# Kernel tuning notes

Hardware: AMD Instinct MI355X
Metric: run time of the kernel (lower is better)

Reference implementation:

```python
import jax, jax.numpy as jnp
import numpy as np

B, C, H, W = 8, 128, 128, 128
R = 4
K = 2 * R + 1  # 9 -> 81 correlation channels


def conv2d(x, w, pad=0):
    return jax.lax.conv_general_dilated(
        x, w, (1, 1), [(pad, pad), (pad, pad)],
        dimension_numbers=('NCHW', 'OIHW', 'NCHW'))


def group_norm(x, gamma, beta, groups, eps=1e-5):
    b, c, h, w = x.shape
    xr = x.reshape(b, groups, c // groups, h, w)
    m = xr.mean(axis=(2, 3, 4), keepdims=True)
    v = ((xr - m) ** 2).mean(axis=(2, 3, 4), keepdims=True)
    xn = ((xr - m) * jax.lax.rsqrt(v + eps)).reshape(b, c, h, w)
    return xn * gamma[None, :, None, None] + beta[None, :, None, None]


def bilinear_warp(x, flow):
    # torch grid_sample(mode=bilinear, padding_mode=zeros, align_corners=True)
    # with vgrid = grid + flow normalized then un-normalized -> pixel coords = grid + flow
    b, c, h, w = x.shape
    px = jnp.arange(w, dtype=flow.dtype)[None, None, :] + flow[:, 0]  # [B,H,W]
    py = jnp.arange(h, dtype=flow.dtype)[None, :, None] + flow[:, 1]
    x0 = jnp.floor(px)
    y0 = jnp.floor(py)
    wx = px - x0
    wy = py - y0

    def sample_one(img, x0, y0, wx, wy):
        def corner(xi, yi):
            valid = ((xi >= 0) & (xi <= w - 1) & (yi >= 0) & (yi <= h - 1)).astype(img.dtype)
            xc = jnp.clip(xi, 0, w - 1).astype(jnp.int32)
            yc = jnp.clip(yi, 0, h - 1).astype(jnp.int32)
            return img[:, yc, xc] * valid[None]  # [C,H,W]
        return (corner(x0, y0) * ((1 - wx) * (1 - wy))[None]
                + corner(x0 + 1, y0) * (wx * (1 - wy))[None]
                + corner(x0, y0 + 1) * ((1 - wx) * wy)[None]
                + corner(x0 + 1, y0 + 1) * (wx * wy)[None])

    return jax.vmap(sample_one)(x, x0, y0, wx, wy)


def cost_volume(f1, f2):
    # 81 shifted windows of zero-padded f2, channel-mean correlation with f1
    b, c, h, w = f1.shape
    pad = jnp.pad(f2, ((0, 0), (0, 0), (R, R), (R, R)))
    vols = [(f1 * jax.lax.slice(pad, (0, 0, y, x), (b, c, y + h, x + w))).mean(axis=1)
            for y in range(K) for x in range(K)]
    return jnp.stack(vols, axis=1)  # [B, 81, H, W]


def _forward(feat1, feat2, p):
    x = conv2d(jnp.concatenate([feat1, feat2], axis=1), p['off_w1'], 1)
    x = jax.nn.silu(group_norm(x, p['off_g1'], p['off_b1'], 32))
    x = conv2d(x, p['off_w2'], 1)
    x = jax.nn.silu(group_norm(x, p['off_g2'], p['off_b2'], 32))
    pred = conv2d(x, p['off_w3'], 1) + p['off_bias3'][None, :, None, None]
    flow = pred[:, :2]
    validity = jax.nn.sigmoid(pred[:, 2:3])
    aligned = bilinear_warp(feat2, flow) * validity
    cv = cost_volume(feat1, aligned)
    diff = jnp.abs(feat1 - aligned)
    ce = jax.nn.relu(group_norm(conv2d(cv, p['corr_w']), p['corr_g'], p['corr_b'], 32))
    de = jax.nn.relu(group_norm(conv2d(diff, p['diff_w']), p['diff_g'], p['diff_b'], 32))
    f = conv2d(jnp.concatenate([ce, de], axis=1), p['fus_w1'], 1)
    f = jax.nn.relu(group_norm(f, p['fus_g1'], p['fus_b1'], 32))
    f = conv2d(f, p['fus_w2'])
    lam = jax.nn.sigmoid(conv2d(f, p['lam_w']) + p['lam_b'][None, :, None, None])
    return aligned, flow, lam


def setup_inputs() -> dict:
    key = jax.random.key(0)
    ks = jax.random.split(key, 12)

    def cw(k, oc, ic, kk, scale=None):
        s = np.float32(np.sqrt(2.0 / (oc * kk * kk))) if scale is None else np.float32(scale)
        return jax.random.normal(k, (oc, ic, kk, kk), jnp.float32) * s

    return {
        'feat1': jax.random.normal(ks[0], (B, C, H, W), jnp.float32),
        'feat2': jax.random.normal(ks[1], (B, C, H, W), jnp.float32),
        'off_w1': cw(ks[2], C, 2 * C, 3),
        'off_g1': jnp.ones((C,), jnp.float32), 'off_b1': jnp.zeros((C,), jnp.float32),
        'off_w2': cw(ks[3], C // 2, C, 3),
        'off_g2': jnp.ones((C // 2,), jnp.float32), 'off_b2': jnp.zeros((C // 2,), jnp.float32),
        'off_w3': cw(ks[4], 3, C // 2, 3, 0.01),  # original inits to zero; small random for nontrivial flow
        'off_bias3': jnp.array([0.0, 0.0, 2.0], jnp.float32),  # bias[2]=2.0 as in _init_weights
        'corr_w': cw(ks[5], C // 2, K * K, 1),
        'corr_g': jnp.ones((C // 2,), jnp.float32), 'corr_b': jnp.zeros((C // 2,), jnp.float32),
        'diff_w': cw(ks[6], C // 2, C, 1),
        'diff_g': jnp.ones((C // 2,), jnp.float32), 'diff_b': jnp.zeros((C // 2,), jnp.float32),
        'fus_w1': cw(ks[7], C, C, 3),
        'fus_g1': jnp.ones((C,), jnp.float32), 'fus_b1': jnp.zeros((C,), jnp.float32),
        'fus_w2': cw(ks[8], C, C, 1),
        'lam_w': cw(ks[9], 1, C, 1),
        'lam_b': jnp.zeros((1,), jnp.float32),
    }


def reference(feat1, feat2, off_w1, off_g1, off_b1, off_w2, off_g2, off_b2, off_w3, off_bias3,
              corr_w, corr_g, corr_b, diff_w, diff_g, diff_b,
              fus_w1, fus_g1, fus_b1, fus_w2, lam_w, lam_b):
    p = dict(off_w1=off_w1, off_g1=off_g1, off_b1=off_b1, off_w2=off_w2, off_g2=off_g2,
             off_b2=off_b2, off_w3=off_w3, off_bias3=off_bias3, corr_w=corr_w, corr_g=corr_g,
             corr_b=corr_b, diff_w=diff_w, diff_g=diff_g, diff_b=diff_b, fus_w1=fus_w1,
             fus_g1=fus_g1, fus_b1=fus_b1, fus_w2=fus_w2, lam_w=lam_w, lam_b=lam_b)
    return _forward(feat1, feat2, p)
```

## Files before the change

### kernel.cpp

```cpp
#include <hip/hip_runtime.h>
#include <math.h>

#define BATCH 8
#define H 128
#define W 128
#define HW 16384

typedef short bf16x8 __attribute__((ext_vector_type(8)));
typedef float f32x16 __attribute__((ext_vector_type(16)));
typedef unsigned int u32;
typedef unsigned short u16;

__device__ __forceinline__ u16 f2bf(float v) {
    u32 u = __float_as_uint(v);
    u = (u + 0x7fffu + ((u >> 16) & 1u)) >> 16;
    return (u16)u;
}

__device__ __forceinline__ void async16(void* lds, const void* g) {
    __builtin_amdgcn_global_load_lds(
        (const __attribute__((address_space(1))) u32*)g,
        (__attribute__((address_space(3))) u32*)lds, 16, 0, 0);
}

__global__ __launch_bounds__(256) void wtrans_kernel(
    const float* __restrict__ w, float* __restrict__ wt, int O, int I, int KK)
{
    int idx = blockIdx.x * 256 + threadIdx.x;
    int total = O * I * KK;
    if (idx >= total) return;
    int k = idx % KK;
    int rest = idx / KK;
    int i = rest % I;
    int o = rest / I;
    wt[(i * KK + k) * O + o] = w[idx];
}

__global__ void wc_kernel(const float* __restrict__ fus_w2,
                          const float* __restrict__ lam_w,
                          float* __restrict__ wc)
{
    int ic = threadIdx.x;
    float s = 0.f;
    for (int oc = 0; oc < 128; ++oc) s += lam_w[oc] * fus_w2[oc * 128 + ic];
    wc[ic] = s;
}

__global__ __launch_bounds__(256) void wprep_kernel(
    const float* __restrict__ w, u16* __restrict__ out, int Cin, int Cout)
{
    int idx = blockIdx.x * 256 + threadIdx.x;
    int total = Cin * 9 * Cout;
    if (idx >= total) return;
    int ocblks = Cout >> 6;
    int pair = idx / 9216;
    int r = idx - pair * 9216;
    int half = r / 4608;
    int r2 = r - half * 4608;
    int kidx = r2 / 512;
    int r3 = r2 - kidx * 512;
    int oc = r3 >> 3;
    int ic8 = r3 & 7;
    int icblk = pair / ocblks;
    int ocblk = pair - icblk * ocblks;
    int ic = icblk * 16 + half * 8 + ic8;
    int o = ocblk * 64 + oc;
    int ky = kidx / 3, kx = kidx - ky * 3;
    out[idx] = f2bf(w[((size_t)(o * Cin + ic) * 3 + ky) * 3 + kx]);
}

__global__ __launch_bounds__(256) void nhwc_concat_kernel(
    const float* __restrict__ f1, const float* __restrict__ f2,
    u16* __restrict__ out)
{
    __shared__ u16 s[32 * 256];
    int tid = threadIdx.x;
    int b = blockIdx.y;
    int xt = blockIdx.x & 3;
    int y = blockIdx.x >> 2;
    int x0 = xt * 32;
    for (int e = tid; e < 8192; e += 256) {
        int c = e >> 5, px = e & 31;
        const float* src = (c < 128) ? f1 + ((size_t)(b * 128 + c)) * HW
                                     : f2 + ((size_t)(b * 128 + c - 128)) * HW;
        s[px * 256 + c] = f2bf(src[y * W + x0 + px]);
    }
    __syncthreads();
    uint4* o4 = (uint4*)(out + (((size_t)b * 130 + y + 1) * 130 + x0 + 1) * 256);
    const uint4* s4 = (const uint4*)s;
    for (int e = tid; e < 1024; e += 256) o4[e] = s4[e];
}

__global__ __launch_bounds__(256) void gn_nhwc_kernel(
    const float* __restrict__ x, const float* __restrict__ gamma,
    const float* __restrict__ beta, const float* __restrict__ stats,
    u16* __restrict__ out, int Csrc, int Cdst, int coff, int Cg, int act)
{
    __shared__ u16 s[32 * 128];
    int tid = threadIdx.x;
    int b = blockIdx.y;
    int xt = blockIdx.x & 3;
    int y = blockIdx.x >> 2;
    int x0 = xt * 32;
    int n = 32 * Csrc;
    for (int e = tid; e < n; e += 256) {
        int c = e >> 5, px = e & 31;
        float v = x[((size_t)(b * Csrc + c)) * HW + y * W + x0 + px];
        int g = c / Cg;
        float mean = stats[(b * 32 + g) * 2];
        float rstd = stats[(b * 32 + g) * 2 + 1];
        float t = (v - mean) * rstd * gamma[c] + beta[c];
        t = (act == 1) ? t / (1.f + expf(-t)) : fmaxf(t, 0.f);
        s[px * Csrc + c] = f2bf(t);
    }
    __syncthreads();
    int cpp = Csrc >> 3;
    int chunks = 32 * cpp;
    for (int e = tid; e < chunks; e += 256) {
        int px = e / cpp, g = e - px * cpp;
        uint4 v = *(const uint4*)&s[px * Csrc + g * 8];
        *(uint4*)&out[(((size_t)b * 130 + y + 1) * 130 + x0 + 1 + px) * Cdst + coff + g * 8] = v;
    }
}

__global__ __launch_bounds__(256, 2) void conv3x3_mfma_kernel(
    const u16* __restrict__ in_nhwc, const u16* __restrict__ wprep,
    float* __restrict__ out, int Cin, int Cout)
{
    __shared__ u16 s_in[2 * 10 * 34 * 8];
    __shared__ u16 s_w[2 * 9 * 64 * 8];

    const int tid = threadIdx.x;
    const int b = blockIdx.y;
    const int x0 = (blockIdx.x & 3) * 32;
    const int y0 = (blockIdx.x >> 2) * 8;
    const int oc0 = blockIdx.z * 64;
    const int ocblks = Cout >> 6;
    const int icblks = Cin >> 4;

    const int lane = tid & 63;
    const int wv = tid >> 6;
    const int m = lane & 31;
    const int hh = lane >> 5;

    f32x16 acc[2][2];
#pragma unroll
    for (int t = 0; t < 2; ++t)
#pragma unroll
        for (int nt = 0; nt < 2; ++nt)
#pragma unroll
            for (int k = 0; k < 16; ++k) acc[t][nt][k] = 0.f;

    const u16* wsrc0 = wprep + (size_t)blockIdx.z * 9216;

    for (int it = 0; it < icblks; ++it) {
        const int ic0 = it * 16;
        __syncthreads();
        for (int e = tid; e < 680; e += 256) {
            int half = (e >= 340);
            int p = e - half * 340;
            int r = p / 34;
            int col = p - r * 34;
            const u16* src = in_nhwc +
                (((size_t)(b * 130 + y0 + r)) * 130 + (x0 + col)) * Cin + ic0 + half * 8;
            async16(&s_in[e * 8], src);
        }
        const u16* wsrc = wsrc0 + (size_t)it * ocblks * 9216;
        for (int e = tid; e < 1152; e += 256)
            async16(&s_w[e * 8], wsrc + e * 8);
        __syncthreads();

#pragma unroll
        for (int kidx = 0; kidx < 9; ++kidx) {
            const int dy = kidx / 3, dx = kidx - dy * 3;
            bf16x8 a0 = *(const bf16x8*)&s_in[(hh * 340 + (wv * 2 + 0 + dy) * 34 + m + dx) * 8];
            bf16x8 a1 = *(const bf16x8*)&s_in[(hh * 340 + (wv * 2 + 1 + dy) * 34 + m + dx) * 8];
            bf16x8 b0 = *(const bf16x8*)&s_w[(hh * 576 + kidx * 64 + m) * 8];
            bf16x8 b1 = *(const bf16x8*)&s_w[(hh * 576 + kidx * 64 + 32 + m) * 8];
            acc[0][0] = __builtin_amdgcn_mfma_f32_32x32x16_bf16(a0, b0, acc[0][0], 0, 0, 0);
            acc[0][1] = __builtin_amdgcn_mfma_f32_32x32x16_bf16(a0, b1, acc[0][1], 0, 0, 0);
            acc[1][0] = __builtin_amdgcn_mfma_f32_32x32x16_bf16(a1, b0, acc[1][0], 0, 0, 0);
            acc[1][1] = __builtin_amdgcn_mfma_f32_32x32x16_bf16(a1, b1, acc[1][1], 0, 0, 0);
        }
    }

#pragma unroll
    for (int t = 0; t < 2; ++t) {
        int y = y0 + wv * 2 + t;
#pragma unroll
        for (int nt = 0; nt < 2; ++nt) {
            int oc = oc0 + nt * 32 + m;
            float* op = out + ((size_t)(b * Cout + oc)) * HW + y * W + x0;
#pragma unroll
            for (int g = 0; g < 4; ++g) {
                float4 v = make_float4(acc[t][nt][g * 4 + 0], acc[t][nt][g * 4 + 1],
                                       acc[t][nt][g * 4 + 2], acc[t][nt][g * 4 + 3]);
                *(float4*)(op + g * 8 + hh * 4) = v;
            }
        }
    }
}

#define CK 8
__global__ __launch_bounds__(256) void conv3x3_kernel(
    const float* __restrict__ in0, int C0,
    const float* __restrict__ in1, int C1,
    const float* __restrict__ wt,
    const float* __restrict__ bias,
    float* __restrict__ out, int Cout)
{
    __shared__ alignas(16) float s_in[CK][6][36];
    __shared__ alignas(16) float s_w[CK][9][32];

    int b = blockIdx.y;
    int octile = blockIdx.z * 32;
    int tile = blockIdx.x;
    int x0 = (tile & 3) * 32;
    int y0 = (tile >> 2) * 4;
    int tid = threadIdx.x;
    int oc4 = (tid & 7) * 4;
    int pg = tid >> 3;
    int tyy = pg >> 3;
    int txx = (pg & 7) * 4;
    int Cin = C0 + C1;

    float acc[4][4];
#pragma unroll
    for (int j = 0; j < 4; ++j)
#pragma unroll
        for (int o = 0; o < 4; ++o) acc[j][o] = 0.f;

    for (int cb = 0; cb < Cin; cb += CK) {
        __syncthreads();
        for (int e = tid; e < CK * 6 * 34; e += 256) {
            int cc = e / 204;
            int rem = e - cc * 204;
            int r = rem / 34;
            int col = rem - r * 34;
            int gy = y0 + r - 1;
            int gx = x0 + col - 1;
            float v = 0.f;
            if (gy >= 0 && gy < H && gx >= 0 && gx < W) {
                int c = cb + cc;
                v = (c < C0) ? in0[((size_t)b * C0 + c) * HW + gy * W + gx]
                             : in1[((size_t)b * C1 + (c - C0)) * HW + gy * W + gx];
            }
            s_in[cc][r][col] = v;
        }
        for (int e = tid; e < CK * 9 * 32; e += 256) {
            int cc = e / 288;
            int rem = e - cc * 288;
            int k = rem / 32;
            int oc = rem - k * 32;
            int gc = octile + oc;
            s_w[cc][k][oc] = (gc < Cout) ? wt[((size_t)(cb + cc) * 9 + k) * Cout + gc] : 0.f;
        }
        __syncthreads();

#pragma unroll
        for (int cc = 0; cc < CK; ++cc) {
            float xin[3][6];
#pragma unroll
            for (int i = 0; i < 3; ++i) {
                const float4 v4 = *(const float4*)&s_in[cc][tyy + i][txx];
                const float2 v2 = *(const float2*)&s_in[cc][tyy + i][txx + 4];
                xin[i][0] = v4.x; xin[i][1] = v4.y; xin[i][2] = v4.z; xin[i][3] = v4.w;
                xin[i][4] = v2.x; xin[i][5] = v2.y;
            }
#pragma unroll
            for (int ky = 0; ky < 3; ++ky)
#pragma unroll
                for (int kx = 0; kx < 3; ++kx) {
                    const float4 wvv = *(const float4*)&s_w[cc][ky * 3 + kx][oc4];
#pragma unroll
                    for (int j = 0; j < 4; ++j) {
                        float xv = xin[ky][j + kx];
                        acc[j][0] += wvv.x * xv;
                        acc[j][1] += wvv.y * xv;
                        acc[j][2] += wvv.z * xv;
                        acc[j][3] += wvv.w * xv;
                    }
                }
        }
    }

    int ox = x0 + txx;
    int oy = y0 + tyy;
#pragma unroll
    for (int o = 0; o < 4; ++o) {
        int oc = octile + oc4 + o;
        if (oc < Cout) {
            float bv = bias ? bias[oc] : 0.f;
            float4 vv = make_float4(acc[0][o] + bv, acc[1][o] + bv,
                                    acc[2][o] + bv, acc[3][o] + bv);
            *(float4*)&out[((size_t)b * Cout + oc) * HW + oy * W + ox] = vv;
        }
    }
}

__global__ __launch_bounds__(256) void gn_stats_kernel(
    const float* __restrict__ x, float* __restrict__ stats, int CgHW)
{
    int bg = blockIdx.x;
    const float4* p4 = (const float4*)(x + (size_t)bg * CgHW);
    int n4 = CgHW / 4;
    float s1 = 0.f, s2 = 0.f;
    for (int i = threadIdx.x; i < n4; i += 256) {
        float4 v = p4[i];
        s1 += v.x + v.y + v.z + v.w;
        s2 += v.x * v.x + v.y * v.y + v.z * v.z + v.w * v.w;
    }
    for (int off = 32; off > 0; off >>= 1) {
        s1 += __shfl_down(s1, off);
        s2 += __shfl_down(s2, off);
    }
    __shared__ float r1[4], r2[4];
    int wid = threadIdx.x >> 6;
    if ((threadIdx.x & 63) == 0) { r1[wid] = s1; r2[wid] = s2; }
    __syncthreads();
    if (threadIdx.x == 0) {
        float a = r1[0] + r1[1] + r1[2] + r1[3];
        float q = r2[0] + r2[1] + r2[2] + r2[3];
        float inv_n = 1.0f / (float)CgHW;
        float mean = a * inv_n;
        float var = q * inv_n - mean * mean;
        stats[bg * 2] = mean;
        stats[bg * 2 + 1] = rsqrtf(var + 1e-5f);
    }
}

__global__ __launch_bounds__(256) void gn_norm_act_kernel(
    const float* __restrict__ x, float* __restrict__ y,
    const float* __restrict__ gamma, const float* __restrict__ beta,
    const float* __restrict__ stats, int C, int Cg, int act)
{
    int idx = blockIdx.x * 256 + threadIdx.x;
    int total4 = BATCH * C * HW / 4;
    if (idx >= total4) return;
    int e = idx * 4;
    int c = (e / HW) % C;
    int b = e / (C * HW);
    int g = c / Cg;
    float mean = stats[(b * 32 + g) * 2];
    float rstd = stats[(b * 32 + g) * 2 + 1];
    float sc = rstd * gamma[c];
    float sh = beta[c] - mean * sc;
    float4 v = ((const float4*)x)[idx];
    float r[4] = {v.x, v.y, v.z, v.w};
#pragma unroll
    for (int i = 0; i < 4; ++i) {
        float t = r[i] * sc + sh;
        if (act == 1) t = t / (1.f + expf(-t));
        else if (act == 2) t = fmaxf(t, 0.f);
        r[i] = t;
    }
    ((float4*)y)[idx] = make_float4(r[0], r[1], r[2], r[3]);
}

__global__ __launch_bounds__(256) void warp_kernel(
    const float* __restrict__ feat2, const float* __restrict__ pred,
    float* __restrict__ aligned, float* __restrict__ flow_out)
{
    int idx = blockIdx.x * 256 + threadIdx.x;
    int b = idx / HW;
    int p = idx - b * HW;
    int y = p >> 7;
    int x = p & 127;
    const float* predb = pred + (size_t)b * 3 * HW;
    float fx = predb[p];
    float fy = predb[HW + p];
    float validity = 1.f / (1.f + expf(-predb[2 * HW + p]));
    flow_out[(size_t)(b * 2) * HW + p] = fx;
    flow_out[(size_t)(b * 2 + 1) * HW + p] = fy;

    float px = (float)x + fx;
    float py = (float)y + fy;
    float x0f = floorf(px), y0f = floorf(py);
    float wx = px - x0f, wy = py - y0f;
    int xi0 = (int)x0f, yi0 = (int)y0f;
    float wgt[2][2] = {{(1.f - wx) * (1.f - wy), wx * (1.f - wy)},
                       {(1.f - wx) * wy, wx * wy}};
    float vm[2][2];
    int offc[2][2];
#pragma unroll
    for (int yy = 0; yy < 2; ++yy)
#pragma unroll
        for (int xx = 0; xx < 2; ++xx) {
            int xi = xi0 + xx, yi = yi0 + yy;
            bool ok = (xi >= 0) && (xi <= W - 1) && (yi >= 0) && (yi <= H - 1);
            vm[yy][xx] = ok ? wgt[yy][xx] : 0.f;
            int xc = min(max(xi, 0), W - 1);
            int yc = min(max(yi, 0), H - 1);
            offc[yy][xx] = yc * W + xc;
        }
    const float* f2b = feat2 + (size_t)b * 128 * HW;
    float* outb = aligned + (size_t)b * 128 * HW;
    for (int c = 0; c < 128; ++c) {
        const float* f2c = f2b + (size_t)c * HW;
        float val = f2c[offc[0][0]] * vm[0][0] + f2c[offc[0][1]] * vm[0][1] +
                    f2c[offc[1][0]] * vm[1][0] + f2c[offc[1][1]] * vm[1][1];
        outb[(size_t)c * HW + p] = val * validity;
    }
}

__global__ __launch_bounds__(256) void costvol_kernel(
    const float* __restrict__ feat1, const float* __restrict__ aligned,
    float* __restrict__ cv)
{
    __shared__ alignas(16) float s_al[24 * 24 * 4];
    int b = blockIdx.y;
    int bx = blockIdx.x & 7, by = blockIdx.x >> 3;
    int tid = threadIdx.x;
    int ly = tid >> 4, lx = tid & 15;
    int gy = by * 16 + ly, gx = bx * 16 + lx;

    float acc[81];
#pragma unroll
    for (int k = 0; k < 81; ++k) acc[k] = 0.f;

    const float* f1b = feat1 + (size_t)b * 128 * HW;
    const float* alb = aligned + (size_t)b * 128 * HW;

    for (int c0 = 0; c0 < 128; c0 += 4) {
        __syncthreads();
        for (int e = tid; e < 24 * 24 * 4; e += 256) {
            int cc = e / 576;
            int rem = e - cc * 576;
            int r = rem / 24;
            int col = rem - r * 24;
            int ay = by * 16 + r - 4, ax = bx * 16 + col - 4;
            float v = 0.f;
            if (ay >= 0 && ay < H && ax >= 0 && ax < W)
                v = alb[(size_t)(c0 + cc) * HW + ay * W + ax];
            s_al[(r * 24 + col) * 4 + cc] = v;
        }
        __syncthreads();
        float f1v[4];
#pragma unroll
        for (int cc = 0; cc < 4; ++cc)
            f1v[cc] = f1b[(size_t)(c0 + cc) * HW + gy * W + gx];
#pragma unroll
        for (int dy = 0; dy < 9; ++dy) {
#pragma unroll
            for (int dx = 0; dx < 9; ++dx) {
                const float4 av = *(const float4*)&s_al[((ly + dy) * 24 + lx + dx) * 4];
                acc[dy * 9 + dx] += av.x * f1v[0] + av.y * f1v[1] + av.z * f1v[2] + av.w * f1v[3];
            }
        }
    }
    const float scale = 1.f / 128.f;
    float* cvb = cv + (size_t)b * 81 * HW + gy * W + gx;
#pragma unroll
    for (int k = 0; k < 81; ++k) cvb[(size_t)k * HW] = acc[k] * scale;
}

__global__ __launch_bounds__(256) void conv1x1_kernel(
    const float* __restrict__ inA, const float* __restrict__ inB,
    const float* __restrict__ wt, float* __restrict__ out, int Cin)
{
    __shared__ alignas(16) float s_w[128 * 64];
    int tid = threadIdx.x;
    for (int e = tid; e < Cin * 64; e += 256) s_w[e] = wt[e];
    __syncthreads();
    int idx = blockIdx.x * 256 + tid;
    int b = idx / HW;
    int p = idx - b * HW;
    float acc[64];
#pragma unroll
    for (int o = 0; o < 64; ++o) acc[o] = 0.f;
    const float* Ab = inA + (size_t)b * Cin * HW + p;
    const float* Bb = inB ? inB + (size_t)b * Cin * HW + p : nullptr;
    for (int ic = 0; ic < Cin; ++ic) {
        float xv = Ab[(size_t)ic * HW];
        if (inB) xv = fabsf(xv - Bb[(size_t)ic * HW]);
        const float* wr = &s_w[ic * 64];
#pragma unroll
        for (int o4 = 0; o4 < 64; o4 += 4) {
            const float4 wvv = *(const float4*)&wr[o4];
            acc[o4 + 0] += wvv.x * xv;
            acc[o4 + 1] += wvv.y * xv;
            acc[o4 + 2] += wvv.z * xv;
            acc[o4 + 3] += wvv.w * xv;
        }
    }
    float* ob = out + (size_t)b * 64 * HW + p;
#pragma unroll
    for (int o = 0; o < 64; ++o) ob[(size_t)o * HW] = acc[o];
}

__global__ __launch_bounds__(256) void lam_kernel(
    const float* __restrict__ f1, const float* __restrict__ wc,
    const float* __restrict__ lam_b, float* __restrict__ out)
{
    __shared__ float s_w[128];
    int tid = threadIdx.x;
    if (tid < 128) s_w[tid] = wc[tid];
    __syncthreads();
    int idx = blockIdx.x * 256 + tid;
    int b = idx / HW;
    int p = idx - b * HW;
    const float* fb = f1 + (size_t)b * 128 * HW + p;
    float acc = 0.f;
#pragma unroll 4
    for (int ic = 0; ic < 128; ++ic) acc += s_w[ic] * fb[(size_t)ic * HW];
    acc += lam_b[0];
    out[idx] = 1.f / (1.f + expf(-acc));
}

extern "C" void kernel_launch(void* const* d_in, const int* in_sizes, int n_in,
                              void* d_out, int out_size, void* d_ws, size_t ws_size,
                              hipStream_t stream)
{
    const float* feat1     = (const float*)d_in[0];
    const float* feat2     = (const float*)d_in[1];
    const float* off_w1    = (const float*)d_in[2];
    const float* off_g1    = (const float*)d_in[3];
    const float* off_b1    = (const float*)d_in[4];
    const float* off_w2    = (const float*)d_in[5];
    const float* off_g2    = (const float*)d_in[6];
    const float* off_b2    = (const float*)d_in[7];
    const float* off_w3    = (const float*)d_in[8];
    const float* off_bias3 = (const float*)d_in[9];
    const float* corr_w    = (const float*)d_in[10];
    const float* corr_g    = (const float*)d_in[11];
    const float* corr_b    = (const float*)d_in[12];
    const float* diff_w    = (const float*)d_in[13];
    const float* diff_g    = (const float*)d_in[14];
    const float* diff_b    = (const float*)d_in[15];
    const float* fus_w1    = (const float*)d_in[16];
    const float* fus_g1    = (const float*)d_in[17];
    const float* fus_b1    = (const float*)d_in[18];
    const float* fus_w2    = (const float*)d_in[19];
    const float* lam_w     = (const float*)d_in[20];
    const float* lam_b     = (const float*)d_in[21];

    float* ws = (float*)d_ws;
    float* x1  = ws;
    float* x2  = ws + 16777216;
    float* Rcv = ws + 25165824;
    float* Rp1 = ws + 35782656;
    u16*  wp1u = (u16*)(ws + 53088256);
    u16*  wp2u = (u16*)(ws + 53235712);
    u16*  wpfu = (u16*)(ws + 53272576);
    float* wT3 = ws + 53346304;
    float* wTc = ws + 53348032;
    float* wTd = ws + 53353216;
    float* wcb = ws + 53361408;
    float* st  = ws + 53361536;

    u16* p1u = (u16*)Rp1;
    u16* p2u = (u16*)Rcv;
    u16* pfu = (u16*)Rcv;
    float* cv = Rcv;
    float* ce = Rp1;
    float* pred = Rp1 + 8388608;

    float* aligned  = (float*)d_out;
    float* flow_out = aligned + 16777216;
    float* lam_out  = aligned + 17039360;

    auto T = [&](const float* w, float* wt, int O, int I, int KK) {
        int total = O * I * KK;
        hipLaunchKernelGGL(wtrans_kernel, dim3((total + 255) / 256), dim3(256), 0, stream,
                           w, wt, O, I, KK);
    };
    T(off_w3, wT3, 3, 64, 9);
    T(corr_w, wTc, 64, 81, 1);
    T(diff_w, wTd, 64, 128, 1);
    hipLaunchKernelGGL(wc_kernel, dim3(1), dim3(128), 0, stream, fus_w2, lam_w, wcb);
    hipLaunchKernelGGL(wprep_kernel, dim3(1152), dim3(256), 0, stream, off_w1, wp1u, 256, 128);
    hipLaunchKernelGGL(wprep_kernel, dim3(288), dim3(256), 0, stream, off_w2, wp2u, 128, 64);
    hipLaunchKernelGGL(wprep_kernel, dim3(576), dim3(256), 0, stream, fus_w1, wpfu, 128, 128);

    hipMemsetAsync(p1u, 0, (size_t)34611200 * 2, stream);
    hipMemsetAsync(p2u, 0, (size_t)17305600 * 2, stream);

    hipLaunchKernelGGL(nhwc_concat_kernel, dim3(512, 8), dim3(256), 0, stream,
                       feat1, feat2, p1u);
    hipLaunchKernelGGL(conv3x3_mfma_kernel, dim3(64, 8, 2), dim3(256), 0, stream,
                       p1u, wp1u, x1, 256, 128);
    hipLaunchKernelGGL(gn_stats_kernel, dim3(256), dim3(256), 0, stream, x1, st, 65536);
    hipLaunchKernelGGL(gn_nhwc_kernel, dim3(512, 8), dim3(256), 0, stream,
                       x1, off_g1, off_b1, st, p2u, 128, 128, 0, 4, 1);
    hipLaunchKernelGGL(conv3x3_mfma_kernel, dim3(64, 8, 1), dim3(256), 0, stream,
                       p2u, wp2u, x2, 128, 64);
    hipLaunchKernelGGL(gn_stats_kernel, dim3(256), dim3(256), 0, stream, x2, st + 512, 32768);
    hipLaunchKernelGGL(gn_norm_act_kernel, dim3(8192), dim3(256), 0, stream,
                       x2, x2, off_g2, off_b2, st + 512, 64, 2, 1);
    hipLaunchKernelGGL(conv3x3_kernel, dim3(128, 8, 1), dim3(256), 0, stream,
                       x2, 64, (const float*)nullptr, 0, wT3, off_bias3, pred, 3);

    hipLaunchKernelGGL(warp_kernel, dim3(512), dim3(256), 0, stream,
                       feat2, pred, aligned, flow_out);
    hipLaunchKernelGGL(costvol_kernel, dim3(64, 8), dim3(256), 0, stream,
                       feat1, aligned, cv);

    hipLaunchKernelGGL(conv1x1_kernel, dim3(512), dim3(256), 0, stream,
                       cv, (const float*)nullptr, wTc, ce, 81);
    hipLaunchKernelGGL(gn_stats_kernel, dim3(256), dim3(256), 0, stream, ce, st + 1024, 32768);
    hipMemsetAsync(pfu, 0, (size_t)17305600 * 2, stream);
    hipLaunchKernelGGL(gn_nhwc_kernel, dim3(512, 8), dim3(256), 0, stream,
                       ce, corr_g, corr_b, st + 1024, pfu, 64, 128, 0, 2, 2);

    hipLaunchKernelGGL(conv1x1_kernel, dim3(512), dim3(256), 0, stream,
                       feat1, aligned, wTd, x2, 128);
    hipLaunchKernelGGL(gn_stats_kernel, dim3(256), dim3(256), 0, stream, x2, st + 1536, 32768);
    hipLaunchKernelGGL(gn_nhwc_kernel, dim3(512, 8), dim3(256), 0, stream,
                       x2, diff_g, diff_b, st + 1536, pfu, 64, 128, 64, 2, 2);

    hipLaunchKernelGGL(conv3x3_mfma_kernel, dim3(64, 8, 2), dim3(256), 0, stream,
                       pfu, wpfu, x1, 128, 128);
    hipLaunchKernelGGL(gn_stats_kernel, dim3(256), dim3(256), 0, stream, x1, st + 2048, 65536);
    hipLaunchKernelGGL(gn_norm_act_kernel, dim3(16384), dim3(256), 0, stream,
                       x1, x1, fus_g1, fus_b1, st + 2048, 128, 4, 2);
    hipLaunchKernelGGL(lam_kernel, dim3(512), dim3(256), 0, stream,
                       x1, wcb, lam_b, lam_out);
}
```

Before: 1.096 ms.

## Enlarge conv tiles with register reuse, bf16 cost volume, border-only zeroing

The MFMA 3x3 conv now computes 16 output rows per block instead of 8. Each wave loads its 6x3 input fragments into registers once and reuses them across the 9 kernel taps and 4 row tiles. The cost volume packs 8 channels per pixel as bf16 in LDS, halving LDS traffic per channel, at the cost of reduced precision in the correlation. Full-buffer memsets of the padded NHWC buffers are replaced by a kernel that zeroes only the 1-pixel border, which avoids writing the whole buffer but relies on the interior being fully overwritten.

```diff
diff --git a/kernel.cpp b/kernel.cpp
--- a/kernel.cpp
+++ b/kernel.cpp
@@ -69,6 +69,26 @@
     out[idx] = f2bf(w[((size_t)(o * Cin + ic) * 3 + ky) * 3 + kx]);
 }
 
+__global__ __launch_bounds__(256) void border_zero_kernel(u16* __restrict__ buf, int C)
+{
+    int chunks = 516 * C / 8;
+    int idx = blockIdx.x * 256 + threadIdx.x;
+    int total = BATCH * chunks;
+    if (idx >= total) return;
+    int b = idx / chunks;
+    int r = idx - b * chunks;
+    int e = r * 8;
+    int pix = e / C;
+    int co = e - pix * C;
+    int y, x;
+    if (pix < 130)      { y = 0;   x = pix; }
+    else if (pix < 260) { y = 129; x = pix - 130; }
+    else if (pix < 388) { y = 1 + (pix - 260); x = 0; }
+    else                { y = 1 + (pix - 388); x = 129; }
+    uint4 z = make_uint4(0u, 0u, 0u, 0u);
+    *(uint4*)&buf[(((size_t)b * 130 + y) * 130 + x) * C + co] = z;
+}
+
 __global__ __launch_bounds__(256) void nhwc_concat_kernel(
     const float* __restrict__ f1, const float* __restrict__ f2,
     u16* __restrict__ out)
@@ -127,13 +147,13 @@
     const u16* __restrict__ in_nhwc, const u16* __restrict__ wprep,
     float* __restrict__ out, int Cin, int Cout)
 {
-    __shared__ u16 s_in[2 * 10 * 34 * 8];
+    __shared__ u16 s_in[2 * 18 * 34 * 8];
     __shared__ u16 s_w[2 * 9 * 64 * 8];
 
     const int tid = threadIdx.x;
     const int b = blockIdx.y;
     const int x0 = (blockIdx.x & 3) * 32;
-    const int y0 = (blockIdx.x >> 2) * 8;
+    const int y0 = (blockIdx.x >> 2) * 16;
     const int oc0 = blockIdx.z * 64;
     const int ocblks = Cout >> 6;
     const int icblks = Cin >> 4;
@@ -143,9 +163,9 @@
     const int m = lane & 31;
     const int hh = lane >> 5;
 
-    f32x16 acc[2][2];
-#pragma unroll
-    for (int t = 0; t < 2; ++t)
+    f32x16 acc[4][2];
+#pragma unroll
+    for (int t = 0; t < 4; ++t)
 #pragma unroll
         for (int nt = 0; nt < 2; ++nt)
 #pragma unroll
@@ -156,9 +176,9 @@
     for (int it = 0; it < icblks; ++it) {
         const int ic0 = it * 16;
         __syncthreads();
-        for (int e = tid; e < 680; e += 256) {
-            int half = (e >= 340);
-            int p = e - half * 340;
+        for (int e = tid; e < 1224; e += 256) {
+            int half = (e >= 612);
+            int p = e - half * 612;
             int r = p / 34;
             int col = p - r * 34;
             const u16* src = in_nhwc +
@@ -170,23 +190,29 @@
             async16(&s_w[e * 8], wsrc + e * 8);
         __syncthreads();
 
+        bf16x8 a[6][3];
+#pragma unroll
+        for (int s = 0; s < 6; ++s)
+#pragma unroll
+            for (int d = 0; d < 3; ++d)
+                a[s][d] = *(const bf16x8*)&s_in[(hh * 612 + (wv * 4 + s) * 34 + m + d) * 8];
+
 #pragma unroll
         for (int kidx = 0; kidx < 9; ++kidx) {
             const int dy = kidx / 3, dx = kidx - dy * 3;
-            bf16x8 a0 = *(const bf16x8*)&s_in[(hh * 340 + (wv * 2 + 0 + dy) * 34 + m + dx) * 8];
-            bf16x8 a1 = *(const bf16x8*)&s_in[(hh * 340 + (wv * 2 + 1 + dy) * 34 + m + dx) * 8];
             bf16x8 b0 = *(const bf16x8*)&s_w[(hh * 576 + kidx * 64 + m) * 8];
             bf16x8 b1 = *(const bf16x8*)&s_w[(hh * 576 + kidx * 64 + 32 + m) * 8];
-            acc[0][0] = __builtin_amdgcn_mfma_f32_32x32x16_bf16(a0, b0, acc[0][0], 0, 0, 0);
-            acc[0][1] = __builtin_amdgcn_mfma_f32_32x32x16_bf16(a0, b1, acc[0][1], 0, 0, 0);
-            acc[1][0] = __builtin_amdgcn_mfma_f32_32x32x16_bf16(a1, b0, acc[1][0], 0, 0, 0);
-            acc[1][1] = __builtin_amdgcn_mfma_f32_32x32x16_bf16(a1, b1, acc[1][1], 0, 0, 0);
-        }
-    }
-
-#pragma unroll
-    for (int t = 0; t < 2; ++t) {
-        int y = y0 + wv * 2 + t;
+#pragma unroll
+            for (int t = 0; t < 4; ++t) {
+                acc[t][0] = __builtin_amdgcn_mfma_f32_32x32x16_bf16(a[t + dy][dx], b0, acc[t][0], 0, 0, 0);
+                acc[t][1] = __builtin_amdgcn_mfma_f32_32x32x16_bf16(a[t + dy][dx], b1, acc[t][1], 0, 0, 0);
+            }
+        }
+    }
+
+#pragma unroll
+    for (int t = 0; t < 4; ++t) {
+        int y = y0 + wv * 4 + t;
 #pragma unroll
         for (int nt = 0; nt < 2; ++nt) {
             int oc = oc0 + nt * 32 + m;
@@ -403,11 +429,11 @@
     }
 }
 
-__global__ __launch_bounds__(256) void costvol_kernel(
+__global__ __launch_bounds__(256, 1) void costvol_kernel(
     const float* __restrict__ feat1, const float* __restrict__ aligned,
     float* __restrict__ cv)
 {
-    __shared__ alignas(16) float s_al[24 * 24 * 4];
+    __shared__ u16 s_al[576 * 8];
     int b = blockIdx.y;
     int bx = blockIdx.x & 7, by = blockIdx.x >> 3;
     int tid = threadIdx.x;
@@ -421,30 +447,46 @@
     const float* f1b = feat1 + (size_t)b * 128 * HW;
     const float* alb = aligned + (size_t)b * 128 * HW;
 
-    for (int c0 = 0; c0 < 128; c0 += 4) {
+    for (int c0 = 0; c0 < 128; c0 += 8) {
         __syncthreads();
-        for (int e = tid; e < 24 * 24 * 4; e += 256) {
-            int cc = e / 576;
-            int rem = e - cc * 576;
-            int r = rem / 24;
-            int col = rem - r * 24;
+        for (int e = tid; e < 576; e += 256) {
+            int r = e / 24;
+            int col = e - r * 24;
             int ay = by * 16 + r - 4, ax = bx * 16 + col - 4;
-            float v = 0.f;
-            if (ay >= 0 && ay < H && ax >= 0 && ax < W)
-                v = alb[(size_t)(c0 + cc) * HW + ay * W + ax];
-            s_al[(r * 24 + col) * 4 + cc] = v;
+            bf16x8 pk;
+            if (ay >= 0 && ay < H && ax >= 0 && ax < W) {
+                const float* src = alb + (size_t)c0 * HW + ay * W + ax;
+#pragma unroll
+                for (int cc = 0; cc < 8; ++cc)
+                    pk[cc] = (short)f2bf(src[(size_t)cc * HW]);
+            } else {
+#pragma unroll
+                for (int cc = 0; cc < 8; ++cc) pk[cc] = 0;
+            }
+            *(bf16x8*)&s_al[e * 8] = pk;
         }
         __syncthreads();
-        float f1v[4];
-#pragma unroll
-        for (int cc = 0; cc < 4; ++cc)
+
+        float f1v[8];
+#pragma unroll
+        for (int cc = 0; cc < 8; ++cc)
             f1v[cc] = f1b[(size_t)(c0 + cc) * HW + gy * W + gx];
+
 #pragma unroll
         for (int dy = 0; dy < 9; ++dy) {
 #pragma unroll
             for (int dx = 0; dx < 9; ++dx) {
-                const float4 av = *(const float4*)&s_al[((ly + dy) * 24 + lx + dx) * 4];
-                acc[dy * 9 + dx] += av.x * f1v[0] + av.y * f1v[1] + av.z * f1v[2] + av.w * f1v[3];
+                union { bf16x8 v; u32 w[4]; } U;
+                U.v = *(const bf16x8*)&s_al[((ly + dy) * 24 + lx + dx) * 8];
+                float s = acc[dy * 9 + dx];
+#pragma unroll
+                for (int q = 0; q < 4; ++q) {
+                    float lo = __uint_as_float(U.w[q] << 16);
+                    float hi = __uint_as_float(U.w[q] & 0xffff0000u);
+                    s += lo * f1v[2 * q];
+                    s += hi * f1v[2 * q + 1];
+                }
+                acc[dy * 9 + dx] = s;
             }
         }
     }
@@ -572,17 +614,17 @@
     hipLaunchKernelGGL(wprep_kernel, dim3(288), dim3(256), 0, stream, off_w2, wp2u, 128, 64);
     hipLaunchKernelGGL(wprep_kernel, dim3(576), dim3(256), 0, stream, fus_w1, wpfu, 128, 128);
 
-    hipMemsetAsync(p1u, 0, (size_t)34611200 * 2, stream);
-    hipMemsetAsync(p2u, 0, (size_t)17305600 * 2, stream);
+    hipLaunchKernelGGL(border_zero_kernel, dim3(516), dim3(256), 0, stream, p1u, 256);
+    hipLaunchKernelGGL(border_zero_kernel, dim3(258), dim3(256), 0, stream, p2u, 128);
 
     hipLaunchKernelGGL(nhwc_concat_kernel, dim3(512, 8), dim3(256), 0, stream,
                        feat1, feat2, p1u);
-    hipLaunchKernelGGL(conv3x3_mfma_kernel, dim3(64, 8, 2), dim3(256), 0, stream,
+    hipLaunchKernelGGL(conv3x3_mfma_kernel, dim3(32, 8, 2), dim3(256), 0, stream,
                        p1u, wp1u, x1, 256, 128);
     hipLaunchKernelGGL(gn_stats_kernel, dim3(256), dim3(256), 0, stream, x1, st, 65536);
     hipLaunchKernelGGL(gn_nhwc_kernel, dim3(512, 8), dim3(256), 0, stream,
                        x1, off_g1, off_b1, st, p2u, 128, 128, 0, 4, 1);
-    hipLaunchKernelGGL(conv3x3_mfma_kernel, dim3(64, 8, 1), dim3(256), 0, stream,
+    hipLaunchKernelGGL(conv3x3_mfma_kernel, dim3(32, 8, 1), dim3(256), 0, stream,
                        p2u, wp2u, x2, 128, 64);
     hipLaunchKernelGGL(gn_stats_kernel, dim3(256), dim3(256), 0, stream, x2, st + 512, 32768);
     hipLaunchKernelGGL(gn_norm_act_kernel, dim3(8192), dim3(256), 0, stream,
@@ -598,7 +640,7 @@
     hipLaunchKernelGGL(conv1x1_kernel, dim3(512), dim3(256), 0, stream,
                        cv, (const float*)nullptr, wTc, ce, 81);
     hipLaunchKernelGGL(gn_stats_kernel, dim3(256), dim3(256), 0, stream, ce, st + 1024, 32768);
-    hipMemsetAsync(pfu, 0, (size_t)17305600 * 2, stream);
+    hipLaunchKernelGGL(border_zero_kernel, dim3(258), dim3(256), 0, stream, pfu, 128);
     hipLaunchKernelGGL(gn_nhwc_kernel, dim3(512, 8), dim3(256), 0, stream,
                        ce, corr_g, corr_b, st + 1024, pfu, 64, 128, 0, 2, 2);
 
@@ -608,7 +650,7 @@
     hipLaunchKernelGGL(gn_nhwc_kernel, dim3(512, 8), dim3(256), 0, stream,
                        x2, diff_g, diff_b, st + 1536, pfu, 64, 128, 64, 2, 2);
 
-    hipLaunchKernelGGL(conv3x3_mfma_kernel, dim3(64, 8, 2), dim3(256), 0, stream,
+    hipLaunchKernelGGL(conv3x3_mfma_kernel, dim3(32, 8, 2), dim3(256), 0, stream,
                        pfu, wpfu, x1, 128, 128);
     hipLaunchKernelGGL(gn_stats_kernel, dim3(256), dim3(256), 0, stream, x1, st + 2048, 65536);
     hipLaunchKernelGGL(gn_norm_act_kernel, dim3(16384), dim3(256), 0, stream,
```

Measured after the change: 1.024 ms. -6.5%, faster.
